# Kernel optimization log

Hardware: AMD Instinct MI355X
Metric: run time of the kernel (lower is better)

## Reference

```python
import jax, jax.numpy as jnp
import numpy as np

N_HEADS = 4
ROPE_THETA = 10000.0


def rotate_half(x):
    h = x.shape[-1] // 2
    return jnp.concatenate([-x[..., h:], x[..., :h]], axis=-1)


def setup_inputs() -> dict:
    key = jax.random.key(0)
    k1, k2, k3, k4, k5 = jax.random.split(key, 5)
    B, L, D, M = 4, 2048, 216, 64
    x = jax.random.normal(k1, (B, L, D), dtype=jnp.float32)
    mem_k = jax.random.normal(k2, (B, M, D), dtype=jnp.float32)
    mem_v = jax.random.normal(k3, (B, M, D), dtype=jnp.float32)
    attention_mask = jnp.ones((B, L), dtype=jnp.int32)
    # pre-transposed Linear weights (y = x @ W); scaled for stability
    Wqkv = jax.random.normal(k4, (D, 3 * D), dtype=jnp.float32) * (D ** -0.5)
    Wo = jax.random.normal(k5, (D, D), dtype=jnp.float32) * (D ** -0.5)
    return {"x": x, "mem_k": mem_k, "mem_v": mem_v,
            "attention_mask": attention_mask, "Wqkv": Wqkv, "Wo": Wo}


def reference(x, mem_k, mem_v, attention_mask, Wqkv, Wo):
    B, L, D = x.shape
    H = N_HEADS
    hd = D // H
    scale = hd ** -0.5
    M = mem_k.shape[1]

    # QKV projection -> [B, L, 3, H, hd] -> [B, H, L, hd]
    qkv = (x @ Wqkv).reshape(B, L, 3, H, hd)
    q = jnp.transpose(qkv[:, :, 0], (0, 2, 1, 3))
    k = jnp.transpose(qkv[:, :, 1], (0, 2, 1, 3))
    v = jnp.transpose(qkv[:, :, 2], (0, 2, 1, 3))

    # RoPE (cos/sin: [L, hd], broadcast over B,H)
    inv_freq = 1.0 / (ROPE_THETA ** (jnp.arange(0, hd, 2, dtype=jnp.float32) / hd))
    t = jnp.arange(L, dtype=jnp.float32)
    freqs = jnp.outer(t, inv_freq)
    emb = jnp.concatenate([freqs, freqs], axis=-1)
    cos, sin = jnp.cos(emb), jnp.sin(emb)
    q = q * cos + rotate_half(q) * sin
    k = k * cos + rotate_half(k) * sin

    # memory KV: [B, M, D] -> [B, H, M, hd], prepend along kv axis
    mk = jnp.transpose(mem_k.reshape(B, M, H, hd), (0, 2, 1, 3))
    mv = jnp.transpose(mem_v.reshape(B, M, H, hd), (0, 2, 1, 3))
    k_all = jnp.concatenate([mk, k], axis=2)  # [B, H, M+L, hd]
    v_all = jnp.concatenate([mv, v], axis=2)

    scores = jnp.einsum('bhld,bhmd->bhlm', q, k_all) * scale  # [B,H,L,M+L]

    # causal mask applies only to the self-attention block (cols >= M)
    causal = jnp.triu(jnp.ones((L, L), dtype=bool), k=1)
    full_causal = jnp.concatenate([jnp.zeros((L, M), dtype=bool), causal], axis=1)
    scores = jnp.where(full_causal[None, None], -jnp.inf, scores)

    # padding mask: memory positions always valid
    combined = jnp.concatenate(
        [jnp.ones((B, M), dtype=attention_mask.dtype), attention_mask], axis=-1)
    scores = jnp.where(combined[:, None, None, :] == 0, -jnp.inf, scores)

    attn = jax.nn.softmax(scores, axis=-1)  # dropout is identity in eval
    out = jnp.einsum('bhlm,bhmd->bhld', attn, v_all)
    out = jnp.transpose(out, (0, 2, 1, 3)).reshape(B, L, D)
    return out @ Wo
```

## Files before the change

kernel.cpp:

```cpp
#include <hip/hip_runtime.h>
#include <math.h>

#define B_ 4
#define L_ 2048
#define D_ 216
#define H_ 4
#define HD 54
#define HDP 64
#define M_ 64
#define LK 2112
#define NT_ 33
#define KP 256
#define SPB 84
#define QSCALE 0.19632593f

typedef __attribute__((ext_vector_type(8))) __bf16 bf16x8;
typedef __attribute__((ext_vector_type(4))) __bf16 bf16x4;
typedef __attribute__((ext_vector_type(4))) float f32x4;

__device__ __forceinline__ int unpack_d(int j) { return (j >> 1) + 27 * (j & 1); }

__global__ __launch_bounds__(256) void prep(const float* __restrict__ Wqkv,
                                            const float* __restrict__ Wo,
                                            const int* __restrict__ amask,
                                            const float* __restrict__ mk,
                                            const float* __restrict__ mv,
                                            __bf16* __restrict__ wqkvt,
                                            __bf16* __restrict__ wot,
                                            float2* __restrict__ table,
                                            float* __restrict__ bias,
                                            int* __restrict__ padflag,
                                            __bf16* __restrict__ kall,
                                            __bf16* __restrict__ vt) {
    const int bid = blockIdx.x, tid = threadIdx.x;
    if (bid < 768) {
        int idx = bid * 256 + tid;
        int pc = idx >> 8, k = idx & 255;
        float v = 0.f;
        if (k < 216) {
            int col = -1;
            if (pc < 256) { int h = pc >> 6, j = pc & 63;
                if (j < HD) col = h * HD + unpack_d(j); }
            else if (pc < 512) { int h = (pc - 256) >> 6, j = (pc - 256) & 63;
                if (j < HD) col = 216 + h * HD + unpack_d(j); }
            else if (pc < 728) col = 432 + (pc - 512);
            if (col >= 0) v = Wqkv[(size_t)k * 648 + col];
        }
        wqkvt[idx] = (__bf16)v;
    } else if (bid < 1024) {
        int idx = (bid - 768) * 256 + tid;
        int n = idx >> 8, k = idx & 255;
        wot[idx] = (__bf16)((n < 216 && k < 216) ? Wo[(size_t)k * 216 + n] : 0.f);
    } else if (bid < 1280) {
        int idx = (bid - 1024) * 256 + tid;
        int l = idx >> 5, ii = idx & 31;
        float2 sc = {0.f, 0.f};
        if (ii < 27) {
            float ang = (float)l * exp2f(-0.49213749924f * (float)ii);
            sc.x = sinf(ang); sc.y = cosf(ang);
        }
        table[idx] = sc;
    } else if (bid < 1313) {
        int idx = (bid - 1280) * 256 + tid;
        if (idx < B_ * LK) {
            int b = idx / LK, c = idx % LK;
            bias[idx] = (c < M_ || amask[b * L_ + c - M_] != 0) ? 0.f : -1e30f;
        }
    } else if (bid == 1313) {
        if (tid < B_ * NT_) {
            int b = tid / NT_, tile = tid % NT_;
            int flag = 0;
            for (int u = 0; u < 64; ++u) {
                int c = tile * 64 + u;
                if (c >= M_ && c < LK && amask[b * L_ + c - M_] == 0) flag = 1;
            }
            padflag[tid] = flag;
        }
    } else {
        int idx = (bid - 1314) * 256 + tid;
        int b  = idx >> 14;
        int m  = (idx >> 8) & 63;
        int h  = (idx >> 6) & 3;
        int dd = idx & 63;
        float kv = (dd < HD) ? mk[((size_t)(b * M_ + m)) * D_ + h * HD + unpack_d(dd)] : 0.f;
        kall[((size_t)(b * 4 + h) * LK + m) * HDP + dd] = (__bf16)kv;
        if (dd < HD)
            vt[((size_t)(b * 4 + h) * HD + dd) * LK + m] =
                (__bf16)mv[((size_t)(b * M_ + m)) * D_ + h * HD + dd];
    }
}

__global__ __launch_bounds__(256) void gemm_qkv(const float* __restrict__ x,
                                                const __bf16* __restrict__ Bt,
                                                const float2* __restrict__ table,
                                                __bf16* __restrict__ qb,
                                                __bf16* __restrict__ kall,
                                                __bf16* __restrict__ vt) {
    __shared__ __align__(16) __bf16 As[8192];
    __shared__ __align__(16) __bf16 Bs[8192];
    const int col0 = blockIdx.x * 128;
    const int row0 = blockIdx.y * 128;
    const int tid = threadIdx.x;
    const int lane = tid & 63;
    const int w = tid >> 6, wm = w >> 1, wn = w & 1;
    const int l15 = lane & 15, l4 = lane >> 4;

    f32x4 acc[4][4];
    #pragma unroll
    for (int m = 0; m < 4; ++m)
        #pragma unroll
        for (int n = 0; n < 4; ++n) acc[m][n] = (f32x4){0.f, 0.f, 0.f, 0.f};

    float4 rfa[4][2];
    bf16x8 rb[4];
    #pragma unroll
    for (int i = 0; i < 4; ++i) { int c = tid + 256 * i, r = c >> 3, c8 = c & 7;
        int k = c8 * 8;
        rfa[i][0] = *reinterpret_cast<const float4*>(x + (size_t)(row0 + r) * 216 + k);
        rfa[i][1] = *reinterpret_cast<const float4*>(x + (size_t)(row0 + r) * 216 + k + 4); }
    #pragma unroll
    for (int i = 0; i < 4; ++i) { int c = tid + 256 * i, r = c >> 3, c8 = c & 7;
        rb[i] = *reinterpret_cast<const bf16x8*>(Bt + (size_t)(col0 + r) * KP + c8 * 8); }

    for (int kit = 0; kit < 4; ++kit) {
        __syncthreads();
        #pragma unroll
        for (int i = 0; i < 4; ++i) { int c = tid + 256 * i, r = c >> 3, c8 = c & 7;
            bf16x8 v;
            #pragma unroll
            for (int j = 0; j < 4; ++j) { v[j] = (__bf16)rfa[i][0][j]; v[4 + j] = (__bf16)rfa[i][1][j]; }
            *reinterpret_cast<bf16x8*>(&As[r * 64 + ((c8 ^ (r & 7)) * 8)]) = v; }
        #pragma unroll
        for (int i = 0; i < 4; ++i) { int c = tid + 256 * i, r = c >> 3, c8 = c & 7;
            *reinterpret_cast<bf16x8*>(&Bs[r * 64 + ((c8 ^ (r & 7)) * 8)]) = rb[i]; }
        __syncthreads();
        if (kit < 3) {
            const int k0 = (kit + 1) * 64;
            #pragma unroll
            for (int i = 0; i < 4; ++i) { int c = tid + 256 * i, r = c >> 3, c8 = c & 7;
                int k = k0 + c8 * 8;
                if (k < 216) {
                    rfa[i][0] = *reinterpret_cast<const float4*>(x + (size_t)(row0 + r) * 216 + k);
                    rfa[i][1] = *reinterpret_cast<const float4*>(x + (size_t)(row0 + r) * 216 + k + 4);
                } else {
                    rfa[i][0] = (float4){0.f, 0.f, 0.f, 0.f};
                    rfa[i][1] = (float4){0.f, 0.f, 0.f, 0.f};
                } }
            #pragma unroll
            for (int i = 0; i < 4; ++i) { int c = tid + 256 * i, r = c >> 3, c8 = c & 7;
                rb[i] = *reinterpret_cast<const bf16x8*>(Bt + (size_t)(col0 + r) * KP + k0 + c8 * 8); }
        }
        #pragma unroll
        for (int ks = 0; ks < 2; ++ks) {
            bf16x8 af[4], bfr[4];
            #pragma unroll
            for (int m = 0; m < 4; ++m) { int row = wm * 64 + m * 16 + l15; int ch = ks * 4 + l4;
                af[m] = *reinterpret_cast<const bf16x8*>(&As[row * 64 + ((ch ^ (row & 7)) * 8)]); }
            #pragma unroll
            for (int n = 0; n < 4; ++n) { int row = wn * 64 + n * 16 + l15; int ch = ks * 4 + l4;
                bfr[n] = *reinterpret_cast<const bf16x8*>(&Bs[row * 64 + ((ch ^ (row & 7)) * 8)]); }
            #pragma unroll
            for (int m = 0; m < 4; ++m)
                #pragma unroll
                for (int n = 0; n < 4; ++n)
                    acc[m][n] = __builtin_amdgcn_mfma_f32_16x16x32_bf16(af[m], bfr[n], acc[m][n], 0, 0, 0);
        }
    }

    #pragma unroll
    for (int m = 0; m < 4; ++m)
        #pragma unroll
        for (int n = 0; n < 4; ++n) {
            const int cc = col0 + wn * 64 + n * 16 + l15;
            const int rowb = row0 + wm * 64 + m * 16 + l4 * 4;
            const int b = rowb >> 11;
            const int lbase = rowb & 2047;
            if (cc < 512) {
                const bool isq = cc < 256;
                const int h = (cc >> 6) & 3, j = cc & 63;
                const int half = j & 1, ii = j >> 1;
                #pragma unroll
                for (int rr = 0; rr < 4; ++rr) {
                    float me = acc[m][n][rr];
                    float pr = __shfl_xor(me, 1);
                    float2 sc = table[(lbase + rr) * 32 + ii];
                    float v = me * sc.y + (half ? pr * sc.x : -pr * sc.x);
                    if (isq) {
                        qb[((size_t)(b * 4 + h) * L_ + lbase + rr) * HDP + j] =
                            (__bf16)(v * QSCALE);
                    } else {
                        kall[((size_t)(b * 4 + h) * LK + M_ + lbase + rr) * HDP + j] =
                            (__bf16)v;
                    }
                }
            } else if (cc < 728) {
                const int dp = cc - 512;
                const int h = (dp * 1214) >> 16;
                const int d = dp - h * 54;
                #pragma unroll
                for (int rr = 0; rr < 4; ++rr)
                    vt[((size_t)(b * 4 + h) * HD + d) * LK + M_ + lbase + rr] =
                        (__bf16)acc[m][n][rr];
            }
        }
}

__global__ __launch_bounds__(256) void gemm_out(const __bf16* __restrict__ A,
                                                const __bf16* __restrict__ Bt,
                                                float* __restrict__ C, int N) {
    __shared__ __align__(16) __bf16 As[8192];
    __shared__ __align__(16) __bf16 Bs[4096];
    const int col0 = blockIdx.x * 64;
    const int row0 = blockIdx.y * 128;
    const int tid = threadIdx.x;
    const int lane = tid & 63;
    const int w = tid >> 6, wm = w >> 1, wn = w & 1;
    const int l15 = lane & 15, l4 = lane >> 4;

    f32x4 acc[4][2];
    #pragma unroll
    for (int m = 0; m < 4; ++m)
        #pragma unroll
        for (int n = 0; n < 2; ++n) acc[m][n] = (f32x4){0.f, 0.f, 0.f, 0.f};

    bf16x8 ra[4], rb[2];
    #pragma unroll
    for (int i = 0; i < 4; ++i) { int c = tid + 256 * i, r = c >> 3, c8 = c & 7;
        ra[i] = *reinterpret_cast<const bf16x8*>(A + (size_t)(row0 + r) * KP + c8 * 8); }
    #pragma unroll
    for (int i = 0; i < 2; ++i) { int c = tid + 256 * i, r = c >> 3, c8 = c & 7;
        rb[i] = *reinterpret_cast<const bf16x8*>(Bt + (size_t)(col0 + r) * KP + c8 * 8); }

    for (int kit = 0; kit < 4; ++kit) {
        __syncthreads();
        #pragma unroll
        for (int i = 0; i < 4; ++i) { int c = tid + 256 * i, r = c >> 3, c8 = c & 7;
            *reinterpret_cast<bf16x8*>(&As[r * 64 + ((c8 ^ (r & 7)) * 8)]) = ra[i]; }
        #pragma unroll
        for (int i = 0; i < 2; ++i) { int c = tid + 256 * i, r = c >> 3, c8 = c & 7;
            *reinterpret_cast<bf16x8*>(&Bs[r * 64 + ((c8 ^ (r & 7)) * 8)]) = rb[i]; }
        __syncthreads();
        if (kit < 3) {
            const int k0 = (kit + 1) * 64;
            #pragma unroll
            for (int i = 0; i < 4; ++i) { int c = tid + 256 * i, r = c >> 3, c8 = c & 7;
                ra[i] = *reinterpret_cast<const bf16x8*>(A + (size_t)(row0 + r) * KP + k0 + c8 * 8); }
            #pragma unroll
            for (int i = 0; i < 2; ++i) { int c = tid + 256 * i, r = c >> 3, c8 = c & 7;
                rb[i] = *reinterpret_cast<const bf16x8*>(Bt + (size_t)(col0 + r) * KP + k0 + c8 * 8); }
        }
        #pragma unroll
        for (int ks = 0; ks < 2; ++ks) {
            bf16x8 af[4], bfr[2];
            #pragma unroll
            for (int m = 0; m < 4; ++m) { int row = wm * 64 + m * 16 + l15; int ch = ks * 4 + l4;
                af[m] = *reinterpret_cast<const bf16x8*>(&As[row * 64 + ((ch ^ (row & 7)) * 8)]); }
            #pragma unroll
            for (int n = 0; n < 2; ++n) { int row = wn * 32 + n * 16 + l15; int ch = ks * 4 + l4;
                bfr[n] = *reinterpret_cast<const bf16x8*>(&Bs[row * 64 + ((ch ^ (row & 7)) * 8)]); }
            #pragma unroll
            for (int m = 0; m < 4; ++m)
                #pragma unroll
                for (int n = 0; n < 2; ++n)
                    acc[m][n] = __builtin_amdgcn_mfma_f32_16x16x32_bf16(af[m], bfr[n], acc[m][n], 0, 0, 0);
        }
    }
    #pragma unroll
    for (int m = 0; m < 4; ++m)
        #pragma unroll
        for (int n = 0; n < 2; ++n) {
            int cc = col0 + wn * 32 + n * 16 + l15;
            if (cc < N) {
                #pragma unroll
                for (int rr = 0; rr < 4; ++rr)
                    C[(size_t)(row0 + wm * 64 + m * 16 + l4 * 4 + rr) * N + cc] = acc[m][n][rr];
            }
        }
}

__global__ __launch_bounds__(256) void flash_split(const __bf16* __restrict__ qb,
                                                   const __bf16* __restrict__ kall,
                                                   const __bf16* __restrict__ vt,
                                                   const float* __restrict__ bias,
                                                   const int* __restrict__ padflag,
                                                   float* __restrict__ op,
                                                   float* __restrict__ ml,
                                                   __bf16* __restrict__ aoutb) {
    int qt = 31, sp = 0;
    {
        int sidx = blockIdx.x, accq = 0;
        for (int q = 0; q < 32; ++q) {
            int c = (q + 9) >> 3;
            if (sidx < accq + c) { qt = q; sp = sidx - accq; break; }
            accq += c;
        }
    }
    const int pb = blockIdx.y * SPB + blockIdx.x;
    const int q0 = qt * 64;
    const int bh = blockIdx.y;
    const int b = bh >> 2, h = bh & 3;
    const int ntl = qt + 2;
    const int ns = (ntl + 7) >> 3;
    const int base = ntl / ns, rem = ntl % ns;
    const int tstart = sp * base + min(sp, rem);
    const int tend = tstart + base + (sp < rem ? 1 : 0);
    const bool single = (ns == 1);

    __shared__ __align__(16) __bf16 Qs[4096];
    __shared__ __align__(16) __bf16 Ks[4096];
    __shared__ __align__(16) __bf16 Vs[4096];
    __shared__ __align__(16) __bf16 Ps[4096];

    const int tid = threadIdx.x;
    const int lane = tid & 63;
    const int w = tid >> 6;
    const int l15 = lane & 15;
    const int l4 = lane >> 4;

    {
        const __bf16* src = qb + ((size_t)bh * L_ + q0) * HDP;
        for (int ch = tid; ch < 512; ch += 256) {
            int row = ch >> 3, c8 = ch & 7;
            bf16x8 v = *reinterpret_cast<const bf16x8*>(src + ch * 8);
            *reinterpret_cast<bf16x8*>(&Qs[row * 64 + ((c8 ^ (row & 7)) * 8)]) = v;
        }
        if (tid < 80) {
            int d = 54 + (tid >> 3), c8 = tid & 7;
            bf16x8 z{};
            *reinterpret_cast<bf16x8*>(&Vs[d * 64 + ((c8 ^ (d & 7)) * 8)]) = z;
        }
    }

    const int rq = q0 + 16 * w + l15;
    const __bf16* kbase = kall + (size_t)bh * LK * HDP;
    const __bf16* vbase = vt + (size_t)bh * HD * LK;

    bf16x8 rk[2], rv[2];
    {
        const __bf16* ks = kbase + (size_t)tstart * 64 * HDP;
        rk[0] = *reinterpret_cast<const bf16x8*>(ks + tid * 8);
        rk[1] = *reinterpret_cast<const bf16x8*>(ks + (tid + 256) * 8);
        { int d = tid >> 3, c8 = tid & 7;
          rv[0] = *reinterpret_cast<const bf16x8*>(vbase + (size_t)d * LK + tstart * 64 + c8 * 8); }
        if (tid < 176) { int c = tid + 256, d = c >> 3, c8 = c & 7;
          rv[1] = *reinterpret_cast<const bf16x8*>(vbase + (size_t)d * LK + tstart * 64 + c8 * 8); }
    }

    __syncthreads();
    bf16x8 aQ[2];
    {
        int qrow = 16 * w + l15, s = (qrow & 7) << 3;
        aQ[0] = *reinterpret_cast<const bf16x8*>(&Qs[qrow * 64 + ((l4 * 8) ^ s)]);
        aQ[1] = *reinterpret_cast<const bf16x8*>(&Qs[qrow * 64 + ((32 + l4 * 8) ^ s)]);
    }

    f32x4 Oacc[4];
    #pragma unroll
    for (int nt = 0; nt < 4; ++nt) Oacc[nt] = (f32x4){0.f, 0.f, 0.f, 0.f};
    float m_run = -1e30f, l_run = 0.f;

    for (int t = tstart; t < tend; ++t) {
        const int cbase = t * 64;
        __syncthreads();
        { int r = tid >> 3, c8 = tid & 7;
          *reinterpret_cast<bf16x8*>(&Ks[r * 64 + ((c8 ^ (r & 7)) * 8)]) = rk[0]; }
        { int c = tid + 256, r = c >> 3, c8 = c & 7;
          *reinterpret_cast<bf16x8*>(&Ks[r * 64 + ((c8 ^ (r & 7)) * 8)]) = rk[1]; }
        { int d = tid >> 3, c8 = tid & 7;
          *reinterpret_cast<bf16x8*>(&Vs[d * 64 + ((c8 ^ (d & 7)) * 8)]) = rv[0]; }
        if (tid < 176) { int c = tid + 256, d = c >> 3, c8 = c & 7;
          *reinterpret_cast<bf16x8*>(&Vs[d * 64 + ((c8 ^ (d & 7)) * 8)]) = rv[1]; }
        __syncthreads();
        if (t + 1 < tend) {
            const __bf16* ks = kbase + (size_t)(cbase + 64) * HDP;
            rk[0] = *reinterpret_cast<const bf16x8*>(ks + tid * 8);
            rk[1] = *reinterpret_cast<const bf16x8*>(ks + (tid + 256) * 8);
            { int d = tid >> 3, c8 = tid & 7;
              rv[0] = *reinterpret_cast<const bf16x8*>(vbase + (size_t)d * LK + cbase + 64 + c8 * 8); }
            if (tid < 176) { int c = tid + 256, d = c >> 3, c8 = c & 7;
              rv[1] = *reinterpret_cast<const bf16x8*>(vbase + (size_t)d * LK + cbase + 64 + c8 * 8); }
        }
        const int flag = padflag[b * NT_ + t];

        f32x4 S[4];
        __builtin_amdgcn_s_setprio(1);
        #pragma unroll
        for (int nt = 0; nt < 4; ++nt) {
            int krow = nt * 16 + l15, s = (krow & 7) << 3;
            bf16x8 b0 = *reinterpret_cast<const bf16x8*>(&Ks[krow * 64 + ((l4 * 8) ^ s)]);
            bf16x8 b1 = *reinterpret_cast<const bf16x8*>(&Ks[krow * 64 + ((32 + l4 * 8) ^ s)]);
            f32x4 acc = (f32x4){0.f, 0.f, 0.f, 0.f};
            acc = __builtin_amdgcn_mfma_f32_16x16x32_bf16(b0, aQ[0], acc, 0, 0, 0);
            acc = __builtin_amdgcn_mfma_f32_16x16x32_bf16(b1, aQ[1], acc, 0, 0, 0);
            S[nt] = acc;
        }
        __builtin_amdgcn_s_setprio(0);
        if (flag) {
            #pragma unroll
            for (int nt = 0; nt < 4; ++nt)
                #pragma unroll
                for (int r = 0; r < 4; ++r)
                    S[nt][r] += bias[b * LK + cbase + nt * 16 + l4 * 4 + r];
        }
        if (t == qt + 1) {
            #pragma unroll
            for (int nt = 0; nt < 4; ++nt)
                #pragma unroll
                for (int r = 0; r < 4; ++r) {
                    int cg = cbase + nt * 16 + l4 * 4 + r;
                    if (cg > rq + M_) S[nt][r] = -1e30f;
                }
        }
        float mx;
        {
            float a0 = fmaxf(fmaxf(S[0][0], S[0][1]), S[0][2]);
            float a1 = fmaxf(fmaxf(S[0][3], S[1][0]), S[1][1]);
            float a2 = fmaxf(fmaxf(S[1][2], S[1][3]), S[2][0]);
            float a3 = fmaxf(fmaxf(S[2][1], S[2][2]), S[2][3]);
            float a4 = fmaxf(fmaxf(S[3][0], S[3][1]), S[3][2]);
            float b0 = fmaxf(fmaxf(a0, a1), a2);
            float b1 = fmaxf(fmaxf(a3, a4), S[3][3]);
            mx = fmaxf(b0, b1);
        }
        mx = fmaxf(mx, __shfl_xor(mx, 16));
        mx = fmaxf(mx, __shfl_xor(mx, 32));
        if (!__all(mx <= m_run + 8.f)) {
            float m_new = fmaxf(m_run, mx);
            float alpha = exp2f(m_run - m_new);
            m_run = m_new;
            l_run *= alpha;
            #pragma unroll
            for (int nt = 0; nt < 4; ++nt)
                #pragma unroll
                for (int r = 0; r < 4; ++r) Oacc[nt][r] *= alpha;
        }
        float ls = 0.f;
        #pragma unroll
        for (int nt = 0; nt < 4; ++nt)
            #pragma unroll
            for (int r = 0; r < 4; ++r) {
                float pv = exp2f(S[nt][r] - m_run);
                S[nt][r] = pv;
                ls += pv;
            }
        ls += __shfl_xor(ls, 16);
        ls += __shfl_xor(ls, 32);
        l_run += ls;
        {
            int prow = 16 * w + l15, s = (prow & 7) << 3;
            #pragma unroll
            for (int nt = 0; nt < 4; ++nt) {
                bf16x4 pk;
                pk[0] = (__bf16)S[nt][0]; pk[1] = (__bf16)S[nt][1];
                pk[2] = (__bf16)S[nt][2]; pk[3] = (__bf16)S[nt][3];
                *reinterpret_cast<bf16x4*>(&Ps[prow * 64 + ((nt * 16 + l4 * 4) ^ s)]) = pk;
            }
        }
        bf16x8 aP[2];
        {
            int prow = 16 * w + l15, s = (prow & 7) << 3;
            aP[0] = *reinterpret_cast<const bf16x8*>(&Ps[prow * 64 + ((l4 * 8) ^ s)]);
            aP[1] = *reinterpret_cast<const bf16x8*>(&Ps[prow * 64 + ((32 + l4 * 8) ^ s)]);
        }
        __builtin_amdgcn_s_setprio(1);
        #pragma unroll
        for (int nt = 0; nt < 4; ++nt) {
            int vrow = nt * 16 + l15, s = (vrow & 7) << 3;
            bf16x8 v0 = *reinterpret_cast<const bf16x8*>(&Vs[vrow * 64 + ((l4 * 8) ^ s)]);
            bf16x8 v1 = *reinterpret_cast<const bf16x8*>(&Vs[vrow * 64 + ((32 + l4 * 8) ^ s)]);
            Oacc[nt] = __builtin_amdgcn_mfma_f32_16x16x32_bf16(v0, aP[0], Oacc[nt], 0, 0, 0);
            Oacc[nt] = __builtin_amdgcn_mfma_f32_16x16x32_bf16(v1, aP[1], Oacc[nt], 0, 0, 0);
        }
        __builtin_amdgcn_s_setprio(0);
    }

    if (single) {
        float inv = 1.f / l_run;
        const size_t rowbase = (size_t)b * L_ + q0 + 16 * w + l15;
        #pragma unroll
        for (int nt = 0; nt < 4; ++nt) {
            #pragma unroll
            for (int r = 0; r < 4; ++r) {
                int d = nt * 16 + l4 * 4 + r;
                if (d < HD)
                    aoutb[rowbase * KP + h * HD + d] = (__bf16)(Oacc[nt][r] * inv);
            }
        }
    } else {
        if (l4 == 0) {
            ml[((size_t)pb * 64 + 16 * w + l15) * 2 + 0] = m_run;
            ml[((size_t)pb * 64 + 16 * w + l15) * 2 + 1] = l_run;
        }
        #pragma unroll
        for (int nt = 0; nt < 4; ++nt) {
            #pragma unroll
            for (int r = 0; r < 4; ++r) {
                int d = nt * 16 + l4 * 4 + r;
                if (d < HD)
                    op[((size_t)pb * HD + d) * 64 + 16 * w + l15] = Oacc[nt][r];
            }
        }
    }
}

__global__ __launch_bounds__(256) void combine(const float* __restrict__ op,
                                               const float* __restrict__ ml,
                                               __bf16* __restrict__ aoutb) {
    const int qt = blockIdx.x + 7, bh = blockIdx.y;
    const int b = bh >> 2, h = bh & 3;
    const int ns = (qt + 9) >> 3;
    int accq = 0;
    for (int q = 0; q < qt; ++q) accq += (q + 9) >> 3;
    const int pb0 = bh * SPB + accq;
    const int row = threadIdx.x & 63;
    const int dseg = threadIdx.x >> 6;

    float mi[5], li[5];
    float m = -1e30f;
    for (int i = 0; i < ns; ++i) {
        mi[i] = ml[((size_t)(pb0 + i) * 64 + row) * 2 + 0];
        li[i] = ml[((size_t)(pb0 + i) * 64 + row) * 2 + 1];
        m = fmaxf(m, mi[i]);
    }
    float wgt[5], Lr = 0.f;
    for (int i = 0; i < ns; ++i) {
        wgt[i] = exp2f(mi[i] - m);
        Lr += li[i] * wgt[i];
    }
    float inv = 1.f / Lr;
    #pragma unroll
    for (int j = 0; j < 14; ++j) {
        int d = dseg * 14 + j;
        if (d < HD) {
            float o = 0.f;
            for (int i = 0; i < ns; ++i)
                o += wgt[i] * op[((size_t)(pb0 + i) * HD + d) * 64 + row];
            aoutb[((size_t)(b * L_) + qt * 64 + row) * KP + h * HD + d] = (__bf16)(o * inv);
        }
    }
}

extern "C" void kernel_launch(void* const* d_in, const int* in_sizes, int n_in,
                              void* d_out, int out_size, void* d_ws, size_t ws_size,
                              hipStream_t stream) {
    const float* x     = (const float*)d_in[0];
    const float* mem_k = (const float*)d_in[1];
    const float* mem_v = (const float*)d_in[2];
    const int*   amask = (const int*)d_in[3];
    const float* Wqkv  = (const float*)d_in[4];
    const float* Wo    = (const float*)d_in[5];
    float* out = (float*)d_out;

    char* p = (char*)d_ws;
    float* bias    = (float*)p;        p += (size_t)B_ * LK * 4;
    int*   padflag = (int*)p;          p += (size_t)B_ * NT_ * 4;
    float2* table  = (float2*)p;       p += (size_t)2048 * 32 * 8;
    __bf16* wqkvt  = (__bf16*)p;       p += (size_t)768 * KP * 2;
    __bf16* wot    = (__bf16*)p;       p += (size_t)256 * KP * 2;
    __bf16* aoutb  = (__bf16*)p;       p += (size_t)8192 * KP * 2;
    __bf16* qb     = (__bf16*)p;       p += (size_t)16 * 2048 * 64 * 2;
    __bf16* kall   = (__bf16*)p;       p += (size_t)16 * 2112 * 64 * 2;
    __bf16* vt     = (__bf16*)p;       p += (size_t)16 * 54 * 2112 * 2;
    float* opbuf   = (float*)p;        p += (size_t)16 * SPB * HD * 64 * 4;
    float* mlbuf   = (float*)p;        p += (size_t)16 * SPB * 64 * 2 * 4;

    prep<<<dim3(1570), 256, 0, stream>>>(Wqkv, Wo, amask, mem_k, mem_v,
                                         wqkvt, wot, table, bias, padflag, kall, vt);
    gemm_qkv<<<dim3(6, 64), 256, 0, stream>>>(x, wqkvt, table, qb, kall, vt);
    flash_split<<<dim3(SPB, 16), 256, 0, stream>>>(qb, kall, vt, bias, padflag,
                                                   opbuf, mlbuf, aoutb);
    combine<<<dim3(25, 16), 256, 0, stream>>>(opbuf, mlbuf, aoutb);
    gemm_out<<<dim3(4, 64), 256, 0, stream>>>(aoutb, wot, out, 216);
}
```

Baseline: 99.15 us.

## Load K/V fragments directly from global memory instead of staging in LDS

The flash attention kernel no longer stages Q, K and V tiles through shared memory with register prefetch and block barriers. Each lane now reads its MFMA operand fragments straight from global or L2. To make the direct V reads uniform, the transposed V buffer is padded from 54 to 64 rows per head, and prep zero-fills the extra rows. This removes the LDS writes and two barriers per tile, but it gives up the software prefetch overlap and adds redundant global reads across the four waves.

```diff
diff --git a/kernel.cpp b/kernel.cpp
--- a/kernel.cpp
+++ b/kernel.cpp
@@ -12,6 +12,7 @@
 #define NT_ 33
 #define KP 256
 #define SPB 84
+#define VTR 64
 #define QSCALE 0.19632593f
 
 typedef __attribute__((ext_vector_type(8))) __bf16 bf16x8;
@@ -76,7 +77,7 @@
             }
             padflag[tid] = flag;
         }
-    } else {
+    } else if (bid < 1570) {
         int idx = (bid - 1314) * 256 + tid;
         int b  = idx >> 14;
         int m  = (idx >> 8) & 63;
@@ -85,8 +86,16 @@
         float kv = (dd < HD) ? mk[((size_t)(b * M_ + m)) * D_ + h * HD + unpack_d(dd)] : 0.f;
         kall[((size_t)(b * 4 + h) * LK + m) * HDP + dd] = (__bf16)kv;
         if (dd < HD)
-            vt[((size_t)(b * 4 + h) * HD + dd) * LK + m] =
+            vt[((size_t)(b * 4 + h) * VTR + dd) * LK + m] =
                 (__bf16)mv[((size_t)(b * M_ + m)) * D_ + h * HD + dd];
+    } else {
+        int idx = (bid - 1570) * 256 + tid;
+        if (idx < 16 * 10 * LK) {
+            int bh = idx / (10 * LK);
+            int r10 = (idx / LK) % 10;
+            int pos = idx % LK;
+            vt[((size_t)bh * VTR + 54 + r10) * LK + pos] = (__bf16)0.f;
+        }
     }
 }
 
@@ -199,7 +208,7 @@
                 const int d = dp - h * 54;
                 #pragma unroll
                 for (int rr = 0; rr < 4; ++rr)
-                    vt[((size_t)(b * 4 + h) * HD + d) * LK + M_ + lbase + rr] =
+                    vt[((size_t)(b * 4 + h) * VTR + d) * LK + M_ + lbase + rr] =
                         (__bf16)acc[m][n][rr];
             }
         }
@@ -306,9 +315,6 @@
     const int tend = tstart + base + (sp < rem ? 1 : 0);
     const bool single = (ns == 1);
 
-    __shared__ __align__(16) __bf16 Qs[4096];
-    __shared__ __align__(16) __bf16 Ks[4096];
-    __shared__ __align__(16) __bf16 Vs[4096];
     __shared__ __align__(16) __bf16 Ps[4096];
 
     const int tid = threadIdx.x;
@@ -317,41 +323,15 @@
     const int l15 = lane & 15;
     const int l4 = lane >> 4;
 
-    {
-        const __bf16* src = qb + ((size_t)bh * L_ + q0) * HDP;
-        for (int ch = tid; ch < 512; ch += 256) {
-            int row = ch >> 3, c8 = ch & 7;
-            bf16x8 v = *reinterpret_cast<const bf16x8*>(src + ch * 8);
-            *reinterpret_cast<bf16x8*>(&Qs[row * 64 + ((c8 ^ (row & 7)) * 8)]) = v;
-        }
-        if (tid < 80) {
-            int d = 54 + (tid >> 3), c8 = tid & 7;
-            bf16x8 z{};
-            *reinterpret_cast<bf16x8*>(&Vs[d * 64 + ((c8 ^ (d & 7)) * 8)]) = z;
-        }
-    }
-
     const int rq = q0 + 16 * w + l15;
     const __bf16* kbase = kall + (size_t)bh * LK * HDP;
-    const __bf16* vbase = vt + (size_t)bh * HD * LK;
-
-    bf16x8 rk[2], rv[2];
-    {
-        const __bf16* ks = kbase + (size_t)tstart * 64 * HDP;
-        rk[0] = *reinterpret_cast<const bf16x8*>(ks + tid * 8);
-        rk[1] = *reinterpret_cast<const bf16x8*>(ks + (tid + 256) * 8);
-        { int d = tid >> 3, c8 = tid & 7;
-          rv[0] = *reinterpret_cast<const bf16x8*>(vbase + (size_t)d * LK + tstart * 64 + c8 * 8); }
-        if (tid < 176) { int c = tid + 256, d = c >> 3, c8 = c & 7;
-          rv[1] = *reinterpret_cast<const bf16x8*>(vbase + (size_t)d * LK + tstart * 64 + c8 * 8); }
-    }
-
-    __syncthreads();
+    const __bf16* vbase = vt + (size_t)bh * VTR * LK;
+
     bf16x8 aQ[2];
     {
-        int qrow = 16 * w + l15, s = (qrow & 7) << 3;
-        aQ[0] = *reinterpret_cast<const bf16x8*>(&Qs[qrow * 64 + ((l4 * 8) ^ s)]);
-        aQ[1] = *reinterpret_cast<const bf16x8*>(&Qs[qrow * 64 + ((32 + l4 * 8) ^ s)]);
+        const __bf16* qp = qb + ((size_t)bh * L_ + q0 + 16 * w + l15) * HDP;
+        aQ[0] = *reinterpret_cast<const bf16x8*>(qp + l4 * 8);
+        aQ[1] = *reinterpret_cast<const bf16x8*>(qp + 32 + l4 * 8);
     }
 
     f32x4 Oacc[4];
@@ -361,34 +341,15 @@
 
     for (int t = tstart; t < tend; ++t) {
         const int cbase = t * 64;
-        __syncthreads();
-        { int r = tid >> 3, c8 = tid & 7;
-          *reinterpret_cast<bf16x8*>(&Ks[r * 64 + ((c8 ^ (r & 7)) * 8)]) = rk[0]; }
-        { int c = tid + 256, r = c >> 3, c8 = c & 7;
-          *reinterpret_cast<bf16x8*>(&Ks[r * 64 + ((c8 ^ (r & 7)) * 8)]) = rk[1]; }
-        { int d = tid >> 3, c8 = tid & 7;
-          *reinterpret_cast<bf16x8*>(&Vs[d * 64 + ((c8 ^ (d & 7)) * 8)]) = rv[0]; }
-        if (tid < 176) { int c = tid + 256, d = c >> 3, c8 = c & 7;
-          *reinterpret_cast<bf16x8*>(&Vs[d * 64 + ((c8 ^ (d & 7)) * 8)]) = rv[1]; }
-        __syncthreads();
-        if (t + 1 < tend) {
-            const __bf16* ks = kbase + (size_t)(cbase + 64) * HDP;
-            rk[0] = *reinterpret_cast<const bf16x8*>(ks + tid * 8);
-            rk[1] = *reinterpret_cast<const bf16x8*>(ks + (tid + 256) * 8);
-            { int d = tid >> 3, c8 = tid & 7;
-              rv[0] = *reinterpret_cast<const bf16x8*>(vbase + (size_t)d * LK + cbase + 64 + c8 * 8); }
-            if (tid < 176) { int c = tid + 256, d = c >> 3, c8 = c & 7;
-              rv[1] = *reinterpret_cast<const bf16x8*>(vbase + (size_t)d * LK + cbase + 64 + c8 * 8); }
-        }
         const int flag = padflag[b * NT_ + t];
 
         f32x4 S[4];
         __builtin_amdgcn_s_setprio(1);
         #pragma unroll
         for (int nt = 0; nt < 4; ++nt) {
-            int krow = nt * 16 + l15, s = (krow & 7) << 3;
-            bf16x8 b0 = *reinterpret_cast<const bf16x8*>(&Ks[krow * 64 + ((l4 * 8) ^ s)]);
-            bf16x8 b1 = *reinterpret_cast<const bf16x8*>(&Ks[krow * 64 + ((32 + l4 * 8) ^ s)]);
+            const __bf16* kp = kbase + (size_t)(cbase + nt * 16 + l15) * HDP;
+            bf16x8 b0 = *reinterpret_cast<const bf16x8*>(kp + l4 * 8);
+            bf16x8 b1 = *reinterpret_cast<const bf16x8*>(kp + 32 + l4 * 8);
             f32x4 acc = (f32x4){0.f, 0.f, 0.f, 0.f};
             acc = __builtin_amdgcn_mfma_f32_16x16x32_bf16(b0, aQ[0], acc, 0, 0, 0);
             acc = __builtin_amdgcn_mfma_f32_16x16x32_bf16(b1, aQ[1], acc, 0, 0, 0);
@@ -465,9 +426,9 @@
         __builtin_amdgcn_s_setprio(1);
         #pragma unroll
         for (int nt = 0; nt < 4; ++nt) {
-            int vrow = nt * 16 + l15, s = (vrow & 7) << 3;
-            bf16x8 v0 = *reinterpret_cast<const bf16x8*>(&Vs[vrow * 64 + ((l4 * 8) ^ s)]);
-            bf16x8 v1 = *reinterpret_cast<const bf16x8*>(&Vs[vrow * 64 + ((32 + l4 * 8) ^ s)]);
+            const __bf16* vp = vbase + (size_t)(nt * 16 + l15) * LK + cbase;
+            bf16x8 v0 = *reinterpret_cast<const bf16x8*>(vp + l4 * 8);
+            bf16x8 v1 = *reinterpret_cast<const bf16x8*>(vp + 32 + l4 * 8);
             Oacc[nt] = __builtin_amdgcn_mfma_f32_16x16x32_bf16(v0, aP[0], Oacc[nt], 0, 0, 0);
             Oacc[nt] = __builtin_amdgcn_mfma_f32_16x16x32_bf16(v1, aP[1], Oacc[nt], 0, 0, 0);
         }
@@ -560,11 +521,11 @@
     __bf16* aoutb  = (__bf16*)p;       p += (size_t)8192 * KP * 2;
     __bf16* qb     = (__bf16*)p;       p += (size_t)16 * 2048 * 64 * 2;
     __bf16* kall   = (__bf16*)p;       p += (size_t)16 * 2112 * 64 * 2;
-    __bf16* vt     = (__bf16*)p;       p += (size_t)16 * 54 * 2112 * 2;
+    __bf16* vt     = (__bf16*)p;       p += (size_t)16 * VTR * 2112 * 2;
     float* opbuf   = (float*)p;        p += (size_t)16 * SPB * HD * 64 * 4;
     float* mlbuf   = (float*)p;        p += (size_t)16 * SPB * 64 * 2 * 4;
 
-    prep<<<dim3(1570), 256, 0, stream>>>(Wqkv, Wo, amask, mem_k, mem_v,
+    prep<<<dim3(2890), 256, 0, stream>>>(Wqkv, Wo, amask, mem_k, mem_v,
                                          wqkvt, wot, table, bias, padflag, kall, vt);
     gemm_qkv<<<dim3(6, 64), 256, 0, stream>>>(x, wqkvt, table, qb, kall, vt);
     flash_split<<<dim3(SPB, 16), 256, 0, stream>>>(qb, kall, vt, bias, padflag,
```

Measured after the change: 159.6 us. 1.61x slower.
